# Performance work log

Measured on AMD Instinct MI355X. Metric: run time of the kernel, lower is better.

## Reference

```python
import jax, jax.numpy as jnp
import numpy as np

N = 50000  # nodes
NEG_SLOPE = 0.2


def gat_conv(x, src, dst, W, a_src, a_dst, b):
    # x: [N, in]; src/dst: [E'] (self-loops already appended)
    h = x @ W                                   # [N, out]
    alpha_s = h @ a_src                         # [N]
    alpha_d = h @ a_dst                         # [N]
    e = alpha_s[src] + alpha_d[dst]             # [E']
    e = jnp.where(e > 0, e, NEG_SLOPE * e)      # leaky_relu
    # segment softmax over destination neighborhoods
    m = jax.ops.segment_max(e, dst, num_segments=N)
    ex = jnp.exp(e - m[dst])
    denom = jax.ops.segment_sum(ex, dst, num_segments=N)
    alpha = ex / denom[dst]                     # [E']
    out = jax.ops.segment_sum(h[src] * alpha[:, None], dst, num_segments=N)
    return out + b


def setup_inputs() -> dict:
    key = jax.random.key(0)
    ks = jax.random.split(key, 16)
    d_in, d_hid, n_cls, E = 256, 256, 32, 400000
    inp = {
        "x": jax.random.normal(ks[0], (N, d_in), jnp.float32),
        "edge_index": jax.random.randint(ks[1], (2, E), 0, N, jnp.int64),
    }
    def glorot(k, shape):
        fan_in, fan_out = shape[0], shape[-1]
        s = jnp.sqrt(6.0 / (fan_in + fan_out))
        return jax.random.uniform(k, shape, jnp.float32, -s, s)
    inp["W0"] = glorot(ks[2], (d_in, d_hid)); inp["as0"] = glorot(ks[3], (1, d_hid))[0]; inp["ad0"] = glorot(ks[4], (1, d_hid))[0]; inp["b0"] = jnp.zeros((d_hid,), jnp.float32)
    inp["W1"] = glorot(ks[5], (d_hid, d_hid)); inp["as1"] = glorot(ks[6], (1, d_hid))[0]; inp["ad1"] = glorot(ks[7], (1, d_hid))[0]; inp["b1"] = jnp.zeros((d_hid,), jnp.float32)
    inp["W2"] = glorot(ks[8], (d_hid, n_cls)); inp["as2"] = glorot(ks[9], (1, n_cls))[0]; inp["ad2"] = glorot(ks[10], (1, n_cls))[0]; inp["b2"] = jnp.zeros((n_cls,), jnp.float32)
    return inp


def reference(x, edge_index, W0, as0, ad0, b0, W1, as1, ad1, b1, W2, as2, ad2, b2):
    # add self-loops (PyG GATConv default)
    loop = jnp.arange(N, dtype=edge_index.dtype)
    src = jnp.concatenate([edge_index[0], loop])
    dst = jnp.concatenate([edge_index[1], loop])
    h = x
    for (W, a_s, a_d, b) in [(W0, as0, ad0, b0), (W1, as1, ad1, b1)]:
        h = gat_conv(h, src, dst, W, a_s, a_d, b)
        h = h * jax.nn.sigmoid(h)  # swish gating
    h = gat_conv(h, src, dst, W2, as2, ad2, b2)
    return jax.nn.log_softmax(h, axis=1)
```

## Files before the change

kernel.cpp:

```cpp
#include <hip/hip_runtime.h>
#include <math.h>

#define N_NODES 50000
#define PAD_ROWS 50176
#define DUAL_BLOCKS 196
#define HALF_OFF (196 * 128)
#define E_RAW   400000
#define E_TOT   (E_RAW + N_NODES)
#define NEG_SLOPE 0.2f

typedef __bf16 bf16_t;
typedef bf16_t bf16x8 __attribute__((ext_vector_type(8)));
typedef bf16_t bf16x4 __attribute__((ext_vector_type(4)));
typedef float  f32x4  __attribute__((ext_vector_type(4)));

__device__ __forceinline__ void gll16(const void* g, void* l) {
    __builtin_amdgcn_global_load_lds(
        (const __attribute__((address_space(1))) void*)g,
        (__attribute__((address_space(3))) void*)l, 16, 0, 0);
}


__global__ void k_hist(const int* __restrict__ ei, int* __restrict__ cnt) {
    int e = blockIdx.x * 256 + threadIdx.x;
    if (e >= E_TOT) return;
    int dst = (e < E_RAW) ? ei[E_RAW + e] : (e - E_RAW);
    atomicAdd(&cnt[dst], 1);
}

__global__ void k_scan1(const int* __restrict__ cnt, int* __restrict__ offs,
                        int* __restrict__ bsum) {
    __shared__ int s[256];
    int i = blockIdx.x * 256 + threadIdx.x;
    int v = (i < N_NODES) ? cnt[i] : 0;
    s[threadIdx.x] = v;
    __syncthreads();
    for (int d = 1; d < 256; d <<= 1) {
        int t = (threadIdx.x >= d) ? s[threadIdx.x - d] : 0;
        __syncthreads();
        s[threadIdx.x] += t;
        __syncthreads();
    }
    if (i < N_NODES) offs[i] = s[threadIdx.x] - v;
    if (threadIdx.x == 255) bsum[blockIdx.x] = s[255];
}

__global__ void k_scan2(int* __restrict__ bsum, int nb) {
    __shared__ int s[256];
    int v = (threadIdx.x < nb) ? bsum[threadIdx.x] : 0;
    s[threadIdx.x] = v;
    __syncthreads();
    for (int d = 1; d < 256; d <<= 1) {
        int t = (threadIdx.x >= d) ? s[threadIdx.x - d] : 0;
        __syncthreads();
        s[threadIdx.x] += t;
        __syncthreads();
    }
    if (threadIdx.x < nb) bsum[threadIdx.x] = s[threadIdx.x] - v;
}

__global__ void k_scan3(int* __restrict__ offs, const int* __restrict__ bsum) {
    int i = blockIdx.x * 256 + threadIdx.x;
    if (i < N_NODES) offs[i] += bsum[blockIdx.x];
}

__global__ void k_scatter(const int* __restrict__ ei, const int* __restrict__ offs,
                          int* __restrict__ cursor, int* __restrict__ srcs) {
    int e = blockIdx.x * 256 + threadIdx.x;
    if (e >= E_TOT) return;
    int src, dst;
    if (e < E_RAW) { src = ei[e]; dst = ei[E_RAW + e]; }
    else           { src = dst = e - E_RAW; }
    int pos = offs[dst] + atomicAdd(&cursor[dst], 1);
    srcs[pos] = src;
}


__global__ void k_split_all(const float* __restrict__ W0, const float* __restrict__ W1,
                            const float* __restrict__ W2,
                            bf16_t* __restrict__ T0h, bf16_t* __restrict__ T0l,
                            bf16_t* __restrict__ T1h, bf16_t* __restrict__ T1l,
                            bf16_t* __restrict__ T2h, bf16_t* __restrict__ T2l) {
    int idx = blockIdx.x * 256 + threadIdx.x;
    float v; bf16_t *ph, *pl; int o;
    if (idx < 65536) {
        int k = idx >> 8, n = idx & 255;
        v = W0[idx]; ph = T0h; pl = T0l; o = n * 256 + k;
    } else if (idx < 131072) {
        int i = idx - 65536;
        int k = i >> 8, n = i & 255;
        v = W1[i]; ph = T1h; pl = T1l; o = n * 256 + k;
    } else {
        int i = idx - 131072;
        int k = i >> 5, n = i & 31;
        v = W2[i]; ph = T2h; pl = T2l; o = n * 256 + k;
    }
    bf16_t h = (bf16_t)v;
    ph[o] = h;
    pl[o] = (bf16_t)(v - (float)h);
}


template<bool A_FP32>
__global__ __launch_bounds__(512) void k_gemm256_dual(
        const float* __restrict__ Af, const bf16_t* __restrict__ Ab,
        const bf16_t* __restrict__ Bth,
        const float* __restrict__ a_s, const float* __restrict__ a_d,
        bf16_t* __restrict__ Hb, float* __restrict__ As, float* __restrict__ Ad) {
    __shared__ __align__(16) bf16_t Bs[16][8][512];

    const int tid  = threadIdx.x;
    const int lane = tid & 63;
    const int w    = tid >> 6;
    const int r16  = lane & 15;
    const int kg   = lane >> 4;

    #pragma unroll
    for (int i = 0; i < 16; ++i) {
        int op   = w * 16 + i;
        int nsub = op >> 3;
        int kk   = op & 7;
        gll16(&Bth[(nsub * 16 + r16) * 256 + kk * 32 + kg * 8], &Bs[nsub][kk][0]);
    }

    const int row0  = blockIdx.x * 128 + w * 16 + r16;
    const int row1  = row0 + HALF_OFF;
    const int rowc0 = min(row0, N_NODES - 1);
    const int rowc1 = min(row1, N_NODES - 1);
    const bool ok0  = row0 < N_NODES;
    const bool ok1  = row1 < N_NODES;

    bf16x8 x0[8], x1[8];
    if constexpr (A_FP32) {
        const float* a0 = Af + rowc0 * 256 + kg * 8;
        const float* a1 = Af + rowc1 * 256 + kg * 8;
        #pragma unroll
        for (int kk = 0; kk < 8; ++kk) {
            float4 v0 = *(const float4*)(a0 + kk * 32);
            float4 v1 = *(const float4*)(a0 + kk * 32 + 4);
            float4 u0 = *(const float4*)(a1 + kk * 32);
            float4 u1 = *(const float4*)(a1 + kk * 32 + 4);
            x0[kk] = bf16x8{(bf16_t)v0.x, (bf16_t)v0.y, (bf16_t)v0.z, (bf16_t)v0.w,
                            (bf16_t)v1.x, (bf16_t)v1.y, (bf16_t)v1.z, (bf16_t)v1.w};
            x1[kk] = bf16x8{(bf16_t)u0.x, (bf16_t)u0.y, (bf16_t)u0.z, (bf16_t)u0.w,
                            (bf16_t)u1.x, (bf16_t)u1.y, (bf16_t)u1.z, (bf16_t)u1.w};
        }
    } else {
        const bf16_t* a0 = Ab + rowc0 * 256 + kg * 8;
        const bf16_t* a1 = Ab + rowc1 * 256 + kg * 8;
        #pragma unroll
        for (int kk = 0; kk < 8; ++kk) {
            x0[kk] = *(const bf16x8*)(a0 + kk * 32);
            x1[kk] = *(const bf16x8*)(a1 + kk * 32);
        }
    }
    __syncthreads();

    f32x4 acc0[16] = {}, acc1[16] = {};
    #pragma unroll
    for (int kk = 0; kk < 8; ++kk) {
        #pragma unroll
        for (int n = 0; n < 16; ++n) {
            bf16x8 wf = *(const bf16x8*)&Bs[n][kk][lane * 8];
            acc0[n] = __builtin_amdgcn_mfma_f32_16x16x32_bf16(wf, x0[kk], acc0[n], 0, 0, 0);
            acc1[n] = __builtin_amdgcn_mfma_f32_16x16x32_bf16(wf, x1[kk], acc1[n], 0, 0, 0);
        }
    }

    {
        float ss = 0.f, sd = 0.f;
        #pragma unroll
        for (int n = 0; n < 16; ++n) {
            f32x4 v = acc0[n];
            if (ok0) {
                bf16x4 st = {(bf16_t)v[0], (bf16_t)v[1], (bf16_t)v[2], (bf16_t)v[3]};
                *(bf16x4*)&Hb[row0 * 256 + n * 16 + kg * 4] = st;
            }
            float4 a4 = *(const float4*)&a_s[n * 16 + kg * 4];
            float4 d4 = *(const float4*)&a_d[n * 16 + kg * 4];
            ss += v[0] * a4.x + v[1] * a4.y + v[2] * a4.z + v[3] * a4.w;
            sd += v[0] * d4.x + v[1] * d4.y + v[2] * d4.z + v[3] * d4.w;
        }
        ss += __shfl_xor(ss, 16); ss += __shfl_xor(ss, 32);
        sd += __shfl_xor(sd, 16); sd += __shfl_xor(sd, 32);
        if (ok0 && kg == 0) { As[row0] = ss; Ad[row0] = sd; }
    }
    {
        float ss = 0.f, sd = 0.f;
        #pragma unroll
        for (int n = 0; n < 16; ++n) {
            f32x4 v = acc1[n];
            if (ok1) {
                bf16x4 st = {(bf16_t)v[0], (bf16_t)v[1], (bf16_t)v[2], (bf16_t)v[3]};
                *(bf16x4*)&Hb[row1 * 256 + n * 16 + kg * 4] = st;
            }
            float4 a4 = *(const float4*)&a_s[n * 16 + kg * 4];
            float4 d4 = *(const float4*)&a_d[n * 16 + kg * 4];
            ss += v[0] * a4.x + v[1] * a4.y + v[2] * a4.z + v[3] * a4.w;
            sd += v[0] * d4.x + v[1] * d4.y + v[2] * d4.z + v[3] * d4.w;
        }
        ss += __shfl_xor(ss, 16); ss += __shfl_xor(ss, 32);
        sd += __shfl_xor(sd, 16); sd += __shfl_xor(sd, 32);
        if (ok1 && kg == 0) { As[row1] = ss; Ad[row1] = sd; }
    }
}


__global__ __launch_bounds__(256) void k_gemm32_mfma(
        const bf16_t* __restrict__ Ab,
        const bf16_t* __restrict__ Bth, const bf16_t* __restrict__ Btl,
        const float* __restrict__ a_s, const float* __restrict__ a_d,
        float* __restrict__ Hc, float* __restrict__ As, float* __restrict__ Ad) {
    const int tid  = threadIdx.x;
    const int lane = tid & 63;
    const int wv   = tid >> 6;
    const int r16  = lane & 15;
    const int kg   = lane >> 4;
    const int rowg = blockIdx.x * 256 + wv * 64;

    int aoff[4], boff[2];
    #pragma unroll
    for (int m = 0; m < 4; ++m) {
        int row = rowg + m * 16 + r16;
        if (row >= N_NODES) row = N_NODES - 1;
        aoff[m] = row * 256 + kg * 8;
    }
    #pragma unroll
    for (int n = 0; n < 2; ++n)
        boff[n] = (n * 16 + r16) * 256 + kg * 8;

    f32x4 accT[2][4] = {};

    #pragma unroll
    for (int kk = 0; kk < 8; ++kk) {
        const int k0 = kk * 32;
        bf16x8 ah[4], bh[2], bl[2];
        #pragma unroll
        for (int m = 0; m < 4; ++m)
            ah[m] = *(const bf16x8*)(Ab + aoff[m] + k0);
        #pragma unroll
        for (int n = 0; n < 2; ++n) {
            bh[n] = *(const bf16x8*)(Bth + boff[n] + k0);
            bl[n] = *(const bf16x8*)(Btl + boff[n] + k0);
        }
        #pragma unroll
        for (int n = 0; n < 2; ++n) {
            #pragma unroll
            for (int m = 0; m < 4; ++m) {
                accT[n][m] = __builtin_amdgcn_mfma_f32_16x16x32_bf16(bh[n], ah[m], accT[n][m], 0, 0, 0);
                accT[n][m] = __builtin_amdgcn_mfma_f32_16x16x32_bf16(bl[n], ah[m], accT[n][m], 0, 0, 0);
            }
        }
    }

    float4 as4[2], ad4[2];
    #pragma unroll
    for (int n = 0; n < 2; ++n) {
        as4[n] = *(const float4*)&a_s[n * 16 + kg * 4];
        ad4[n] = *(const float4*)&a_d[n * 16 + kg * 4];
    }
    #pragma unroll
    for (int m = 0; m < 4; ++m) {
        int row = rowg + m * 16 + r16;
        bool ok = row < N_NODES;
        float ss = 0.f, sd = 0.f;
        #pragma unroll
        for (int n = 0; n < 2; ++n) {
            f32x4 v = accT[n][m];
            if (ok) {
                float4 st = {v[0], v[1], v[2], v[3]};
                *(float4*)&Hc[row * 32 + n * 16 + kg * 4] = st;
            }
            ss += v[0] * as4[n].x + v[1] * as4[n].y + v[2] * as4[n].z + v[3] * as4[n].w;
            sd += v[0] * ad4[n].x + v[1] * ad4[n].y + v[2] * ad4[n].z + v[3] * ad4[n].w;
        }
        ss += __shfl_xor(ss, 16); ss += __shfl_xor(ss, 32);
        sd += __shfl_xor(sd, 16); sd += __shfl_xor(sd, 32);
        if (ok && kg == 0) { As[row] = ss; Ad[row] = sd; }
    }
}


__global__ __launch_bounds__(256) void k_attn(
        const float* __restrict__ As, const float* __restrict__ Ad,
        const int* __restrict__ offs, const int* __restrict__ cnts,
        const int* __restrict__ srcs,
        int2* __restrict__ meta, float* __restrict__ inv) {
    const int lane  = threadIdx.x & 63;
    const int wv    = threadIdx.x >> 6;
    const int g     = lane >> 3;
    const int gl    = lane & 7;
    const int node  = (blockIdx.x * 4 + wv) * 8 + g;
    if (node >= N_NODES) return;
    const int start = offs[node];
    const int cnt   = cnts[node];
    const float ad  = Ad[node];

    float m = -1e30f;
    for (int i = gl; i < cnt; i += 8) {
        float e = As[srcs[start + i]] + ad;
        e = e > 0.f ? e : NEG_SLOPE * e;
        m = fmaxf(m, e);
    }
    m = fmaxf(m, __shfl_xor(m, 1));
    m = fmaxf(m, __shfl_xor(m, 2));
    m = fmaxf(m, __shfl_xor(m, 4));

    float denom = 0.f;
    for (int i = gl; i < cnt; i += 8) {
        int s = srcs[start + i];
        float e = As[s] + ad;
        e = e > 0.f ? e : NEG_SLOPE * e;
        float p = __expf(e - m);
        denom += p;
        meta[start + i] = make_int2(s, __float_as_int(p));
    }
    denom += __shfl_xor(denom, 1);
    denom += __shfl_xor(denom, 2);
    denom += __shfl_xor(denom, 4);
    if (gl == 0) inv[node] = 1.f / denom;
}


__global__ __launch_bounds__(256) void k_gather256(
        const bf16_t* __restrict__ Hb, const int2* __restrict__ meta,
        const int* __restrict__ offs, const int* __restrict__ cnts,
        const float* __restrict__ inv,
        const float* __restrict__ bias, bf16_t* __restrict__ Hout) {
    const int gl   = threadIdx.x & 31;
    const int node = blockIdx.x * 8 + (threadIdx.x >> 5);
    if (node >= N_NODES) return;
    const int start = offs[node];
    const int cnt   = cnts[node];
    const float iv  = inv[node];
    const int c0 = gl * 8;

    float acc[8] = {};
    for (int j = 0; j < cnt; j += 4) {
        int2 mp[4];
        #pragma unroll
        for (int k = 0; k < 4; ++k) mp[k] = meta[start + j + k];
        #pragma unroll
        for (int k = 0; k < 4; ++k) {
            float p = (j + k < cnt) ? __int_as_float(mp[k].y) : 0.f;
            bf16x8 hv = *(const bf16x8*)&Hb[mp[k].x * 256 + c0];
            #pragma unroll
            for (int q = 0; q < 8; ++q) acc[q] += p * (float)hv[q];
        }
    }

    float4 b0 = *(const float4*)&bias[c0];
    float4 b1 = *(const float4*)&bias[c0 + 4];
    float bb[8] = {b0.x, b0.y, b0.z, b0.w, b1.x, b1.y, b1.z, b1.w};
    bf16x8 st;
    #pragma unroll
    for (int q = 0; q < 8; ++q) {
        float v = acc[q] * iv + bb[q];
        v = v / (1.f + __expf(-v));
        st[q] = (bf16_t)v;
    }
    *(bf16x8*)&Hout[node * 256 + c0] = st;
}


__global__ __launch_bounds__(256) void k_gather_final(
        const float* __restrict__ Hc,
        const int2* __restrict__ meta,
        const int* __restrict__ offs, const int* __restrict__ cnts,
        const float* __restrict__ inv,
        const float* __restrict__ bias, float* __restrict__ out) {
    const int gl   = threadIdx.x & 31;
    const int node = blockIdx.x * 8 + (threadIdx.x >> 5);
    if (node >= N_NODES) return;
    const int start = offs[node];
    const int cnt   = cnts[node];
    const float iv  = inv[node];

    float acc = 0.f;
    for (int j = 0; j < cnt; j += 4) {
        int2 mp[4];
        #pragma unroll
        for (int k = 0; k < 4; ++k) mp[k] = meta[start + j + k];
        #pragma unroll
        for (int k = 0; k < 4; ++k) {
            float p = (j + k < cnt) ? __int_as_float(mp[k].y) : 0.f;
            acc += p * Hc[mp[k].x * 32 + gl];
        }
    }

    float v = acc * iv + bias[gl];
    float mm = v;
    #pragma unroll
    for (int o = 16; o; o >>= 1) mm = fmaxf(mm, __shfl_xor(mm, o));
    float ex = __expf(v - mm), sum = ex;
    #pragma unroll
    for (int o = 16; o; o >>= 1) sum += __shfl_xor(sum, o);
    out[node * 32 + gl] = v - mm - __logf(sum);
}


extern "C" void kernel_launch(void* const* d_in, const int* in_sizes, int n_in,
                              void* d_out, int out_size, void* d_ws, size_t ws_size,
                              hipStream_t stream) {
    const float* x   = (const float*)d_in[0];
    const int*   ei  = (const int*)  d_in[1];
    const float* W0  = (const float*)d_in[2];
    const float* as0 = (const float*)d_in[3];
    const float* ad0 = (const float*)d_in[4];
    const float* b0  = (const float*)d_in[5];
    const float* W1  = (const float*)d_in[6];
    const float* as1 = (const float*)d_in[7];
    const float* ad1 = (const float*)d_in[8];
    const float* b1  = (const float*)d_in[9];
    const float* W2  = (const float*)d_in[10];
    const float* as2 = (const float*)d_in[11];
    const float* ad2 = (const float*)d_in[12];
    const float* b2  = (const float*)d_in[13];
    float* out = (float*)d_out;

    char* ws = (char*)d_ws;
    bf16_t* hA_b  = (bf16_t*)(ws + 0);
    bf16_t* hB_b  = (bf16_t*)(ws + 25690112);
    float*  hC    = (float*) (ws + 51380224);
    float*  As    = (float*) (ws + 57780224);
    float*  Ad    = (float*) (ws + 57980224);
    float*  inv   = (float*) (ws + 58180224);
    int*    cnts  = (int*)   (ws + 58380224);
    int*    cursor= (int*)   (ws + 58580224);
    int*    offs  = (int*)   (ws + 58780224);
    int*    srcs  = (int*)   (ws + 58980224);
    int2*   meta  = (int2*)  (ws + 60780224);
    int*    bsum  = (int*)   (ws + 64380260 + 28);
    bf16_t* Wth0  = (bf16_t*)(ws + 64381312);
    bf16_t* Wtl0  = (bf16_t*)(ws + 64512384);
    bf16_t* Wth1  = (bf16_t*)(ws + 64643456);
    bf16_t* Wtl1  = (bf16_t*)(ws + 64774528);
    bf16_t* Wth2  = (bf16_t*)(ws + 64905600);
    bf16_t* Wtl2  = (bf16_t*)(ws + 64921984);

    const int NB = (N_NODES + 255) / 256;

    hipMemsetAsync(cnts, 0, 400000, stream);
    hipMemsetAsync((char*)meta + (size_t)E_TOT * 8, 0, 32, stream);

    k_hist     <<<(E_TOT + 255) / 256, 256, 0, stream>>>(ei, cnts);
    k_scan1    <<<NB, 256, 0, stream>>>(cnts, offs, bsum);
    k_scan2    <<<1, 256, 0, stream>>>(bsum, NB);
    k_scan3    <<<NB, 256, 0, stream>>>(offs, bsum);
    k_scatter  <<<(E_TOT + 255) / 256, 256, 0, stream>>>(ei, offs, cursor, srcs);
    k_split_all<<<544, 256, 0, stream>>>(W0, W1, W2, Wth0, Wtl0, Wth1, Wtl1, Wth2, Wtl2);

    const int GATHER_BLOCKS = (N_NODES + 7) / 8;
    const int ATTN_BLOCKS   = (N_NODES + 31) / 32;

    k_gemm256_dual<true><<<DUAL_BLOCKS, 512, 0, stream>>>(x, nullptr, Wth0, as0, ad0, hA_b, As, Ad);
    k_attn<<<ATTN_BLOCKS, 256, 0, stream>>>(As, Ad, offs, cnts, srcs, meta, inv);
    k_gather256<<<GATHER_BLOCKS, 256, 0, stream>>>(hA_b, meta, offs, cnts, inv, b0, hB_b);
    k_gemm256_dual<false><<<DUAL_BLOCKS, 512, 0, stream>>>(nullptr, hB_b, Wth1, as1, ad1, hA_b, As, Ad);
    k_attn<<<ATTN_BLOCKS, 256, 0, stream>>>(As, Ad, offs, cnts, srcs, meta, inv);
    k_gather256<<<GATHER_BLOCKS, 256, 0, stream>>>(hA_b, meta, offs, cnts, inv, b1, hB_b);
    k_gemm32_mfma<<<NB, 256, 0, stream>>>(hB_b, Wth2, Wtl2, as2, ad2, hC, As, Ad);
    k_attn<<<ATTN_BLOCKS, 256, 0, stream>>>(As, Ad, offs, cnts, srcs, meta, inv);
    k_gather_final<<<GATHER_BLOCKS, 256, 0, stream>>>(hC, meta, offs, cnts, inv, b2, out);
}
```

Baseline: 237.1 us.

## Split layer-1 GEMM across column halves and fold memsets into kernels

Adds a column-split variant of the 256-wide GEMM for layer 1, launching twice as many blocks, each computing 128 output columns with half the shared memory. Each half writes partial attention-score sums to separate buffers, and the attention kernel adds the two partials. Separately, the two hipMemsetAsync calls are replaced by zeroing inside k_split_all and k_scatter, removing two launches. In exchange, every block re-reads the A rows and the attention kernel does extra loads.

New measurement: 236.6 us. Within noise of the previous version (-0.2%).

```diff
diff --git a/kernel.cpp b/kernel.cpp
--- a/kernel.cpp
+++ b/kernel.cpp
@@ -65,8 +65,10 @@
 }
 
 __global__ void k_scatter(const int* __restrict__ ei, const int* __restrict__ offs,
-                          int* __restrict__ cursor, int* __restrict__ srcs) {
+                          int* __restrict__ cursor, int* __restrict__ srcs,
+                          int2* __restrict__ meta) {
     int e = blockIdx.x * 256 + threadIdx.x;
+    if (e < 4) meta[E_TOT + e] = make_int2(0, 0);
     if (e >= E_TOT) return;
     int src, dst;
     if (e < E_RAW) { src = ei[e]; dst = ei[E_RAW + e]; }
@@ -80,8 +82,10 @@
                             const float* __restrict__ W2,
                             bf16_t* __restrict__ T0h, bf16_t* __restrict__ T0l,
                             bf16_t* __restrict__ T1h, bf16_t* __restrict__ T1l,
-                            bf16_t* __restrict__ T2h, bf16_t* __restrict__ T2l) {
+                            bf16_t* __restrict__ T2h, bf16_t* __restrict__ T2l,
+                            int* __restrict__ cnts, int* __restrict__ cursor) {
     int idx = blockIdx.x * 256 + threadIdx.x;
+    if (idx < N_NODES) { cnts[idx] = 0; cursor[idx] = 0; }
     float v; bf16_t *ph, *pl; int o;
     if (idx < 65536) {
         int k = idx >> 8, n = idx & 255;
@@ -90,11 +94,11 @@
         int i = idx - 65536;
         int k = i >> 8, n = i & 255;
         v = W1[i]; ph = T1h; pl = T1l; o = n * 256 + k;
-    } else {
+    } else if (idx < 139264) {
         int i = idx - 131072;
         int k = i >> 5, n = i & 31;
         v = W2[i]; ph = T2h; pl = T2l; o = n * 256 + k;
-    }
+    } else return;
     bf16_t h = (bf16_t)v;
     ph[o] = h;
     pl[o] = (bf16_t)(v - (float)h);
@@ -202,6 +206,102 @@
         ss += __shfl_xor(ss, 16); ss += __shfl_xor(ss, 32);
         sd += __shfl_xor(sd, 16); sd += __shfl_xor(sd, 32);
         if (ok1 && kg == 0) { As[row1] = ss; Ad[row1] = sd; }
+    }
+}
+
+
+__global__ __launch_bounds__(512) void k_gemm256_cs(
+        const bf16_t* __restrict__ Ab, const bf16_t* __restrict__ Bth,
+        const float* __restrict__ a_s, const float* __restrict__ a_d,
+        bf16_t* __restrict__ Hb,
+        float* __restrict__ As0, float* __restrict__ Ad0,
+        float* __restrict__ As1, float* __restrict__ Ad1) {
+    __shared__ __align__(16) bf16_t Bs[8][8][512];
+
+    const int pair = blockIdx.x >> 1;
+    const int ch   = blockIdx.x & 1;
+    const int tid  = threadIdx.x;
+    const int lane = tid & 63;
+    const int w    = tid >> 6;
+    const int r16  = lane & 15;
+    const int kg   = lane >> 4;
+    const int cbase = ch * 128;
+
+    #pragma unroll
+    for (int i = 0; i < 8; ++i) {
+        int op   = w * 8 + i;
+        int nsub = op >> 3;
+        int kk   = op & 7;
+        gll16(&Bth[(cbase + nsub * 16 + r16) * 256 + kk * 32 + kg * 8], &Bs[nsub][kk][0]);
+    }
+
+    const int row0  = pair * 128 + w * 16 + r16;
+    const int row1  = row0 + HALF_OFF;
+    const int rowc0 = min(row0, N_NODES - 1);
+    const int rowc1 = min(row1, N_NODES - 1);
+    const bool ok0  = row0 < N_NODES;
+    const bool ok1  = row1 < N_NODES;
+
+    bf16x8 x0[8], x1[8];
+    {
+        const bf16_t* a0 = Ab + rowc0 * 256 + kg * 8;
+        const bf16_t* a1 = Ab + rowc1 * 256 + kg * 8;
+        #pragma unroll
+        for (int kk = 0; kk < 8; ++kk) {
+            x0[kk] = *(const bf16x8*)(a0 + kk * 32);
+            x1[kk] = *(const bf16x8*)(a1 + kk * 32);
+        }
+    }
+    __syncthreads();
+
+    f32x4 acc0[8] = {}, acc1[8] = {};
+    #pragma unroll
+    for (int kk = 0; kk < 8; ++kk) {
+        #pragma unroll
+        for (int n = 0; n < 8; ++n) {
+            bf16x8 wf = *(const bf16x8*)&Bs[n][kk][lane * 8];
+            acc0[n] = __builtin_amdgcn_mfma_f32_16x16x32_bf16(wf, x0[kk], acc0[n], 0, 0, 0);
+            acc1[n] = __builtin_amdgcn_mfma_f32_16x16x32_bf16(wf, x1[kk], acc1[n], 0, 0, 0);
+        }
+    }
+
+    float* Asp = ch ? As1 : As0;
+    float* Adp = ch ? Ad1 : Ad0;
+    {
+        float ss = 0.f, sd = 0.f;
+        #pragma unroll
+        for (int n = 0; n < 8; ++n) {
+            f32x4 v = acc0[n];
+            if (ok0) {
+                bf16x4 st = {(bf16_t)v[0], (bf16_t)v[1], (bf16_t)v[2], (bf16_t)v[3]};
+                *(bf16x4*)&Hb[row0 * 256 + cbase + n * 16 + kg * 4] = st;
+            }
+            float4 a4 = *(const float4*)&a_s[cbase + n * 16 + kg * 4];
+            float4 d4 = *(const float4*)&a_d[cbase + n * 16 + kg * 4];
+            ss += v[0] * a4.x + v[1] * a4.y + v[2] * a4.z + v[3] * a4.w;
+            sd += v[0] * d4.x + v[1] * d4.y + v[2] * d4.z + v[3] * d4.w;
+        }
+        ss += __shfl_xor(ss, 16); ss += __shfl_xor(ss, 32);
+        sd += __shfl_xor(sd, 16); sd += __shfl_xor(sd, 32);
+        if (ok0 && kg == 0) { Asp[row0] = ss; Adp[row0] = sd; }
+    }
+    {
+        float ss = 0.f, sd = 0.f;
+        #pragma unroll
+        for (int n = 0; n < 8; ++n) {
+            f32x4 v = acc1[n];
+            if (ok1) {
+                bf16x4 st = {(bf16_t)v[0], (bf16_t)v[1], (bf16_t)v[2], (bf16_t)v[3]};
+                *(bf16x4*)&Hb[row1 * 256 + cbase + n * 16 + kg * 4] = st;
+            }
+            float4 a4 = *(const float4*)&a_s[cbase + n * 16 + kg * 4];
+            float4 d4 = *(const float4*)&a_d[cbase + n * 16 + kg * 4];
+            ss += v[0] * a4.x + v[1] * a4.y + v[2] * a4.z + v[3] * a4.w;
+            sd += v[0] * d4.x + v[1] * d4.y + v[2] * d4.z + v[3] * d4.w;
+        }
+        ss += __shfl_xor(ss, 16); ss += __shfl_xor(ss, 32);
+        sd += __shfl_xor(sd, 16); sd += __shfl_xor(sd, 32);
+        if (ok1 && kg == 0) { Asp[row1] = ss; Adp[row1] = sd; }
     }
 }
 
@@ -282,7 +382,9 @@
 
 
 __global__ __launch_bounds__(256) void k_attn(
-        const float* __restrict__ As, const float* __restrict__ Ad,
+        const float* __restrict__ As0, const float* __restrict__ Ad0,
+        const float* __restrict__ As1, const float* __restrict__ Ad1,
+        const int dual,
         const int* __restrict__ offs, const int* __restrict__ cnts,
         const int* __restrict__ srcs,
         int2* __restrict__ meta, float* __restrict__ inv) {
@@ -294,11 +396,15 @@
     if (node >= N_NODES) return;
     const int start = offs[node];
     const int cnt   = cnts[node];
-    const float ad  = Ad[node];
+    float ad = Ad0[node];
+    if (dual) ad += Ad1[node];
 
     float m = -1e30f;
     for (int i = gl; i < cnt; i += 8) {
-        float e = As[srcs[start + i]] + ad;
+        int s = srcs[start + i];
+        float as = As0[s];
+        if (dual) as += As1[s];
+        float e = as + ad;
         e = e > 0.f ? e : NEG_SLOPE * e;
         m = fmaxf(m, e);
     }
@@ -309,7 +415,9 @@
     float denom = 0.f;
     for (int i = gl; i < cnt; i += 8) {
         int s = srcs[start + i];
-        float e = As[s] + ad;
+        float as = As0[s];
+        if (dual) as += As1[s];
+        float e = as + ad;
         e = e > 0.f ? e : NEG_SLOPE * e;
         float p = __expf(e - m);
         denom += p;
@@ -430,36 +538,36 @@
     int*    offs  = (int*)   (ws + 58780224);
     int*    srcs  = (int*)   (ws + 58980224);
     int2*   meta  = (int2*)  (ws + 60780224);
-    int*    bsum  = (int*)   (ws + 64380260 + 28);
+    int*    bsum  = (int*)   (ws + 64380288);
     bf16_t* Wth0  = (bf16_t*)(ws + 64381312);
     bf16_t* Wtl0  = (bf16_t*)(ws + 64512384);
     bf16_t* Wth1  = (bf16_t*)(ws + 64643456);
     bf16_t* Wtl1  = (bf16_t*)(ws + 64774528);
     bf16_t* Wth2  = (bf16_t*)(ws + 64905600);
     bf16_t* Wtl2  = (bf16_t*)(ws + 64921984);
+    float*  As1p  = (float*) (ws + 64938368);
+    float*  Ad1p  = (float*) (ws + 65138368);
 
     const int NB = (N_NODES + 255) / 256;
 
-    hipMemsetAsync(cnts, 0, 400000, stream);
-    hipMemsetAsync((char*)meta + (size_t)E_TOT * 8, 0, 32, stream);
-
-    k_hist     <<<(E_TOT + 255) / 256, 256, 0, stream>>>(ei, cnts);
-    k_scan1    <<<NB, 256, 0, stream>>>(cnts, offs, bsum);
-    k_scan2    <<<1, 256, 0, stream>>>(bsum, NB);
-    k_scan3    <<<NB, 256, 0, stream>>>(offs, bsum);
-    k_scatter  <<<(E_TOT + 255) / 256, 256, 0, stream>>>(ei, offs, cursor, srcs);
-    k_split_all<<<544, 256, 0, stream>>>(W0, W1, W2, Wth0, Wtl0, Wth1, Wtl1, Wth2, Wtl2);
+    k_split_all<<<544, 256, 0, stream>>>(W0, W1, W2, Wth0, Wtl0, Wth1, Wtl1,
+                                         Wth2, Wtl2, cnts, cursor);
+    k_hist   <<<(E_TOT + 255) / 256, 256, 0, stream>>>(ei, cnts);
+    k_scan1  <<<NB, 256, 0, stream>>>(cnts, offs, bsum);
+    k_scan2  <<<1, 256, 0, stream>>>(bsum, NB);
+    k_scan3  <<<NB, 256, 0, stream>>>(offs, bsum);
+    k_scatter<<<(E_TOT + 255) / 256, 256, 0, stream>>>(ei, offs, cursor, srcs, meta);
 
     const int GATHER_BLOCKS = (N_NODES + 7) / 8;
     const int ATTN_BLOCKS   = (N_NODES + 31) / 32;
 
     k_gemm256_dual<true><<<DUAL_BLOCKS, 512, 0, stream>>>(x, nullptr, Wth0, as0, ad0, hA_b, As, Ad);
-    k_attn<<<ATTN_BLOCKS, 256, 0, stream>>>(As, Ad, offs, cnts, srcs, meta, inv);
+    k_attn<<<ATTN_BLOCKS, 256, 0, stream>>>(As, Ad, As, Ad, 0, offs, cnts, srcs, meta, inv);
     k_gather256<<<GATHER_BLOCKS, 256, 0, stream>>>(hA_b, meta, offs, cnts, inv, b0, hB_b);
-    k_gemm256_dual<false><<<DUAL_BLOCKS, 512, 0, stream>>>(nullptr, hB_b, Wth1, as1, ad1, hA_b, As, Ad);
-    k_attn<<<ATTN_BLOCKS, 256, 0, stream>>>(As, Ad, offs, cnts, srcs, meta, inv);
+    k_gemm256_cs<<<DUAL_BLOCKS * 2, 512, 0, stream>>>(hB_b, Wth1, as1, ad1, hA_b, As, Ad, As1p, Ad1p);
+    k_attn<<<ATTN_BLOCKS, 256, 0, stream>>>(As, Ad, As1p, Ad1p, 1, offs, cnts, srcs, meta, inv);
     k_gather256<<<GATHER_BLOCKS, 256, 0, stream>>>(hA_b, meta, offs, cnts, inv, b1, hB_b);
     k_gemm32_mfma<<<NB, 256, 0, stream>>>(hB_b, Wth2, Wtl2, as2, ad2, hC, As, Ad);
-    k_attn<<<ATTN_BLOCKS, 256, 0, stream>>>(As, Ad, offs, cnts, srcs, meta, inv);
+    k_attn<<<ATTN_BLOCKS, 256, 0, stream>>>(As, Ad, As, Ad, 0, offs, cnts, srcs, meta, inv);
     k_gather_final<<<GATHER_BLOCKS, 256, 0, stream>>>(hC, meta, offs, cnts, inv, b2, out);
 }
```

## Fuse attention softmax into gather kernels and merge scan/memset launches

Applied to the files above, without the earlier changes.

Removes the separate k_attn pass by computing leaky-relu attention weights and the softmax denominator inline inside each gather kernel. The max subtraction is dropped, so exp is taken on unnormalized logits. The 256-wide gather now handles two nodes per 32-lane group to add memory-level parallelism. It also folds scan2/scan3 into one kernel and replaces the memsets with zeroing inside k_split_all, cutting launch count and the meta/inv round trips through memory. Risks are overflow in exp without the max shift, and divergence when the two paired nodes have different degrees.

New measurement: 232.4 us. 2.0% less time.

```diff
diff --git a/kernel.cpp b/kernel.cpp
--- a/kernel.cpp
+++ b/kernel.cpp
@@ -45,7 +45,8 @@
     if (threadIdx.x == 255) bsum[blockIdx.x] = s[255];
 }
 
-__global__ void k_scan2(int* __restrict__ bsum, int nb) {
+__global__ void k_scan23(int* __restrict__ offs, const int* __restrict__ bsum,
+                         int nb) {
     __shared__ int s[256];
     int v = (threadIdx.x < nb) ? bsum[threadIdx.x] : 0;
     s[threadIdx.x] = v;
@@ -56,17 +57,15 @@
         s[threadIdx.x] += t;
         __syncthreads();
     }
-    if (threadIdx.x < nb) bsum[threadIdx.x] = s[threadIdx.x] - v;
-}
-
-__global__ void k_scan3(int* __restrict__ offs, const int* __restrict__ bsum) {
+    int add = (blockIdx.x == 0) ? 0 : s[blockIdx.x - 1];
     int i = blockIdx.x * 256 + threadIdx.x;
-    if (i < N_NODES) offs[i] += bsum[blockIdx.x];
+    if (i < N_NODES) offs[i] += add;
 }
 
 __global__ void k_scatter(const int* __restrict__ ei, const int* __restrict__ offs,
                           int* __restrict__ cursor, int* __restrict__ srcs) {
     int e = blockIdx.x * 256 + threadIdx.x;
+    if (e < 64) srcs[E_TOT + e] = 0;
     if (e >= E_TOT) return;
     int src, dst;
     if (e < E_RAW) { src = ei[e]; dst = ei[E_RAW + e]; }
@@ -80,8 +79,10 @@
                             const float* __restrict__ W2,
                             bf16_t* __restrict__ T0h, bf16_t* __restrict__ T0l,
                             bf16_t* __restrict__ T1h, bf16_t* __restrict__ T1l,
-                            bf16_t* __restrict__ T2h, bf16_t* __restrict__ T2l) {
+                            bf16_t* __restrict__ T2h, bf16_t* __restrict__ T2l,
+                            int* __restrict__ cnts, int* __restrict__ cursor) {
     int idx = blockIdx.x * 256 + threadIdx.x;
+    if (idx < N_NODES) { cnts[idx] = 0; cursor[idx] = 0; }
     float v; bf16_t *ph, *pl; int o;
     if (idx < 65536) {
         int k = idx >> 8, n = idx & 255;
@@ -90,11 +91,11 @@
         int i = idx - 65536;
         int k = i >> 8, n = i & 255;
         v = W1[i]; ph = T1h; pl = T1l; o = n * 256 + k;
-    } else {
+    } else if (idx < 139264) {
         int i = idx - 131072;
         int k = i >> 5, n = i & 31;
         v = W2[i]; ph = T2h; pl = T2l; o = n * 256 + k;
-    }
+    } else return;
     bf16_t h = (bf16_t)v;
     ph[o] = h;
     pl[o] = (bf16_t)(v - (float)h);
@@ -281,114 +282,119 @@
 }
 
 
-__global__ __launch_bounds__(256) void k_attn(
+__global__ __launch_bounds__(256) void k_gather256_f(
+        const bf16_t* __restrict__ Hb,
         const float* __restrict__ As, const float* __restrict__ Ad,
         const int* __restrict__ offs, const int* __restrict__ cnts,
         const int* __restrict__ srcs,
-        int2* __restrict__ meta, float* __restrict__ inv) {
-    const int lane  = threadIdx.x & 63;
-    const int wv    = threadIdx.x >> 6;
-    const int g     = lane >> 3;
-    const int gl    = lane & 7;
-    const int node  = (blockIdx.x * 4 + wv) * 8 + g;
-    if (node >= N_NODES) return;
-    const int start = offs[node];
-    const int cnt   = cnts[node];
-    const float ad  = Ad[node];
-
-    float m = -1e30f;
-    for (int i = gl; i < cnt; i += 8) {
-        float e = As[srcs[start + i]] + ad;
-        e = e > 0.f ? e : NEG_SLOPE * e;
-        m = fmaxf(m, e);
-    }
-    m = fmaxf(m, __shfl_xor(m, 1));
-    m = fmaxf(m, __shfl_xor(m, 2));
-    m = fmaxf(m, __shfl_xor(m, 4));
-
-    float denom = 0.f;
-    for (int i = gl; i < cnt; i += 8) {
-        int s = srcs[start + i];
-        float e = As[s] + ad;
-        e = e > 0.f ? e : NEG_SLOPE * e;
-        float p = __expf(e - m);
-        denom += p;
-        meta[start + i] = make_int2(s, __float_as_int(p));
-    }
-    denom += __shfl_xor(denom, 1);
-    denom += __shfl_xor(denom, 2);
-    denom += __shfl_xor(denom, 4);
-    if (gl == 0) inv[node] = 1.f / denom;
-}
-
-
-__global__ __launch_bounds__(256) void k_gather256(
-        const bf16_t* __restrict__ Hb, const int2* __restrict__ meta,
-        const int* __restrict__ offs, const int* __restrict__ cnts,
-        const float* __restrict__ inv,
         const float* __restrict__ bias, bf16_t* __restrict__ Hout) {
-    const int gl   = threadIdx.x & 31;
-    const int node = blockIdx.x * 8 + (threadIdx.x >> 5);
-    if (node >= N_NODES) return;
-    const int start = offs[node];
-    const int cnt   = cnts[node];
-    const float iv  = inv[node];
+    const int gl = threadIdx.x & 31;
+    const int hw = blockIdx.x * 8 + (threadIdx.x >> 5);
+    const int n0 = hw * 2, n1 = n0 + 1;
+    if (n0 >= N_NODES) return;
+    const bool has1 = n1 < N_NODES;
+    const int st0 = offs[n0], c0n = cnts[n0];
+    const int st1 = has1 ? offs[n1] : st0;
+    const int c1n = has1 ? cnts[n1] : 0;
+    const float ad0 = Ad[n0];
+    const float ad1 = has1 ? Ad[n1] : 0.f;
     const int c0 = gl * 8;
 
-    float acc[8] = {};
-    for (int j = 0; j < cnt; j += 4) {
-        int2 mp[4];
-        #pragma unroll
-        for (int k = 0; k < 4; ++k) mp[k] = meta[start + j + k];
+    float acc0[8] = {}, acc1[8] = {};
+    float den0 = 0.f, den1 = 0.f;
+    const int jmax = max(c0n, c1n);
+    for (int j = 0; j < jmax; j += 4) {
+        int s0[4], s1[4];
         #pragma unroll
         for (int k = 0; k < 4; ++k) {
-            float p = (j + k < cnt) ? __int_as_float(mp[k].y) : 0.f;
-            bf16x8 hv = *(const bf16x8*)&Hb[mp[k].x * 256 + c0];
-            #pragma unroll
-            for (int q = 0; q < 8; ++q) acc[q] += p * (float)hv[q];
+            s0[k] = srcs[st0 + j + k];
+            s1[k] = srcs[st1 + j + k];
+        }
+        #pragma unroll
+        for (int k = 0; k < 4; ++k) {
+            if (j + k < c0n) {
+                int s = s0[k];
+                float e = As[s] + ad0;
+                e = e > 0.f ? e : NEG_SLOPE * e;
+                float p = __expf(e);
+                den0 += p;
+                bf16x8 hv = *(const bf16x8*)&Hb[s * 256 + c0];
+                #pragma unroll
+                for (int q = 0; q < 8; ++q) acc0[q] += p * (float)hv[q];
+            }
+            if (j + k < c1n) {
+                int s = s1[k];
+                float e = As[s] + ad1;
+                e = e > 0.f ? e : NEG_SLOPE * e;
+                float p = __expf(e);
+                den1 += p;
+                bf16x8 hv = *(const bf16x8*)&Hb[s * 256 + c0];
+                #pragma unroll
+                for (int q = 0; q < 8; ++q) acc1[q] += p * (float)hv[q];
+            }
         }
     }
 
     float4 b0 = *(const float4*)&bias[c0];
     float4 b1 = *(const float4*)&bias[c0 + 4];
     float bb[8] = {b0.x, b0.y, b0.z, b0.w, b1.x, b1.y, b1.z, b1.w};
-    bf16x8 st;
-    #pragma unroll
-    for (int q = 0; q < 8; ++q) {
-        float v = acc[q] * iv + bb[q];
-        v = v / (1.f + __expf(-v));
-        st[q] = (bf16_t)v;
-    }
-    *(bf16x8*)&Hout[node * 256 + c0] = st;
-}
-
-
-__global__ __launch_bounds__(256) void k_gather_final(
+    {
+        const float iv = 1.f / den0;
+        bf16x8 st;
+        #pragma unroll
+        for (int q = 0; q < 8; ++q) {
+            float v = acc0[q] * iv + bb[q];
+            v = v / (1.f + __expf(-v));
+            st[q] = (bf16_t)v;
+        }
+        *(bf16x8*)&Hout[n0 * 256 + c0] = st;
+    }
+    if (has1) {
+        const float iv = 1.f / den1;
+        bf16x8 st;
+        #pragma unroll
+        for (int q = 0; q < 8; ++q) {
+            float v = acc1[q] * iv + bb[q];
+            v = v / (1.f + __expf(-v));
+            st[q] = (bf16_t)v;
+        }
+        *(bf16x8*)&Hout[n1 * 256 + c0] = st;
+    }
+}
+
+
+__global__ __launch_bounds__(256) void k_gather_final_f(
         const float* __restrict__ Hc,
-        const int2* __restrict__ meta,
+        const float* __restrict__ As, const float* __restrict__ Ad,
         const int* __restrict__ offs, const int* __restrict__ cnts,
-        const float* __restrict__ inv,
+        const int* __restrict__ srcs,
         const float* __restrict__ bias, float* __restrict__ out) {
     const int gl   = threadIdx.x & 31;
     const int node = blockIdx.x * 8 + (threadIdx.x >> 5);
     if (node >= N_NODES) return;
     const int start = offs[node];
     const int cnt   = cnts[node];
-    const float iv  = inv[node];
-
-    float acc = 0.f;
+    const float ad  = Ad[node];
+
+    float acc = 0.f, denom = 0.f;
     for (int j = 0; j < cnt; j += 4) {
-        int2 mp[4];
-        #pragma unroll
-        for (int k = 0; k < 4; ++k) mp[k] = meta[start + j + k];
+        int s4[4];
+        #pragma unroll
+        for (int k = 0; k < 4; ++k) s4[k] = srcs[start + j + k];
         #pragma unroll
         for (int k = 0; k < 4; ++k) {
-            float p = (j + k < cnt) ? __int_as_float(mp[k].y) : 0.f;
-            acc += p * Hc[mp[k].x * 32 + gl];
-        }
-    }
-
-    float v = acc * iv + bias[gl];
+            if (j + k < cnt) {
+                int s = s4[k];
+                float e = As[s] + ad;
+                e = e > 0.f ? e : NEG_SLOPE * e;
+                float p = __expf(e);
+                denom += p;
+                acc += p * Hc[s * 32 + gl];
+            }
+        }
+    }
+
+    float v = acc / denom + bias[gl];
     float mm = v;
     #pragma unroll
     for (int o = 16; o; o >>= 1) mm = fmaxf(mm, __shfl_xor(mm, o));
@@ -424,42 +430,34 @@
     float*  hC    = (float*) (ws + 51380224);
     float*  As    = (float*) (ws + 57780224);
     float*  Ad    = (float*) (ws + 57980224);
-    float*  inv   = (float*) (ws + 58180224);
-    int*    cnts  = (int*)   (ws + 58380224);
-    int*    cursor= (int*)   (ws + 58580224);
-    int*    offs  = (int*)   (ws + 58780224);
-    int*    srcs  = (int*)   (ws + 58980224);
-    int2*   meta  = (int2*)  (ws + 60780224);
-    int*    bsum  = (int*)   (ws + 64380260 + 28);
-    bf16_t* Wth0  = (bf16_t*)(ws + 64381312);
-    bf16_t* Wtl0  = (bf16_t*)(ws + 64512384);
-    bf16_t* Wth1  = (bf16_t*)(ws + 64643456);
-    bf16_t* Wtl1  = (bf16_t*)(ws + 64774528);
-    bf16_t* Wth2  = (bf16_t*)(ws + 64905600);
-    bf16_t* Wtl2  = (bf16_t*)(ws + 64921984);
+    int*    cnts  = (int*)   (ws + 58180224);
+    int*    cursor= (int*)   (ws + 58380224);
+    int*    offs  = (int*)   (ws + 58580224);
+    int*    srcs  = (int*)   (ws + 58780224);
+    int*    bsum  = (int*)   (ws + 60580480);
+    bf16_t* Wth0  = (bf16_t*)(ws + 60581504);
+    bf16_t* Wtl0  = (bf16_t*)(ws + 60712576);
+    bf16_t* Wth1  = (bf16_t*)(ws + 60843648);
+    bf16_t* Wtl1  = (bf16_t*)(ws + 60974720);
+    bf16_t* Wth2  = (bf16_t*)(ws + 61105792);
+    bf16_t* Wtl2  = (bf16_t*)(ws + 61122176);
 
     const int NB = (N_NODES + 255) / 256;
 
-    hipMemsetAsync(cnts, 0, 400000, stream);
-    hipMemsetAsync((char*)meta + (size_t)E_TOT * 8, 0, 32, stream);
-
-    k_hist     <<<(E_TOT + 255) / 256, 256, 0, stream>>>(ei, cnts);
-    k_scan1    <<<NB, 256, 0, stream>>>(cnts, offs, bsum);
-    k_scan2    <<<1, 256, 0, stream>>>(bsum, NB);
-    k_scan3    <<<NB, 256, 0, stream>>>(offs, bsum);
-    k_scatter  <<<(E_TOT + 255) / 256, 256, 0, stream>>>(ei, offs, cursor, srcs);
-    k_split_all<<<544, 256, 0, stream>>>(W0, W1, W2, Wth0, Wtl0, Wth1, Wtl1, Wth2, Wtl2);
-
-    const int GATHER_BLOCKS = (N_NODES + 7) / 8;
-    const int ATTN_BLOCKS   = (N_NODES + 31) / 32;
+    k_split_all<<<544, 256, 0, stream>>>(W0, W1, W2, Wth0, Wtl0, Wth1, Wtl1,
+                                         Wth2, Wtl2, cnts, cursor);
+    k_hist   <<<(E_TOT + 255) / 256, 256, 0, stream>>>(ei, cnts);
+    k_scan1  <<<NB, 256, 0, stream>>>(cnts, offs, bsum);
+    k_scan23 <<<NB, 256, 0, stream>>>(offs, bsum, NB);
+    k_scatter<<<(E_TOT + 255) / 256, 256, 0, stream>>>(ei, offs, cursor, srcs);
+
+    const int GATHER2_BLOCKS = (N_NODES + 15) / 16;
+    const int FINAL_BLOCKS   = (N_NODES + 7) / 8;
 
     k_gemm256_dual<true><<<DUAL_BLOCKS, 512, 0, stream>>>(x, nullptr, Wth0, as0, ad0, hA_b, As, Ad);
-    k_attn<<<ATTN_BLOCKS, 256, 0, stream>>>(As, Ad, offs, cnts, srcs, meta, inv);
-    k_gather256<<<GATHER_BLOCKS, 256, 0, stream>>>(hA_b, meta, offs, cnts, inv, b0, hB_b);
+    k_gather256_f<<<GATHER2_BLOCKS, 256, 0, stream>>>(hA_b, As, Ad, offs, cnts, srcs, b0, hB_b);
     k_gemm256_dual<false><<<DUAL_BLOCKS, 512, 0, stream>>>(nullptr, hB_b, Wth1, as1, ad1, hA_b, As, Ad);
-    k_attn<<<ATTN_BLOCKS, 256, 0, stream>>>(As, Ad, offs, cnts, srcs, meta, inv);
-    k_gather256<<<GATHER_BLOCKS, 256, 0, stream>>>(hA_b, meta, offs, cnts, inv, b1, hB_b);
+    k_gather256_f<<<GATHER2_BLOCKS, 256, 0, stream>>>(hA_b, As, Ad, offs, cnts, srcs, b1, hB_b);
     k_gemm32_mfma<<<NB, 256, 0, stream>>>(hB_b, Wth2, Wtl2, as2, ad2, hC, As, Ad);
-    k_attn<<<ATTN_BLOCKS, 256, 0, stream>>>(As, Ad, offs, cnts, srcs, meta, inv);
-    k_gather_final<<<GATHER_BLOCKS, 256, 0, stream>>>(hC, meta, offs, cnts, inv, b2, out);
-}
+    k_gather_final_f<<<FINAL_BLOCKS, 256, 0, stream>>>(hC, As, Ad, offs, cnts, srcs, b2, out);
+}
```
